# Kernel optimization log

Measured on AMD Instinct MI355X. Metric: run time of the kernel, lower is better.

The kernel has to match this reference:

```python
import jax, jax.numpy as jnp
import numpy as np

N_NODES = 50000
N_EDGES = 600000
IN_CH = 128
HID_CH = 128
OUT_CH = 64
NUM_GRAPHS = 512


def _gcn_conv(x, W, b, src, dst, n):
    # PyG GCNConv (eval): h = D^{-1/2} (A + I) D^{-1/2} (x W) + b
    h = x @ W  # [N, C]
    loop = jnp.arange(n)
    s = jnp.concatenate([src, loop])  # add self-loops
    d = jnp.concatenate([dst, loop])
    deg = jax.ops.segment_sum(jnp.ones_like(d, dtype=h.dtype), d, num_segments=n)
    dinv = jnp.where(deg > 0, jax.lax.rsqrt(deg), 0.0)
    coef = dinv[s] * dinv[d]  # [E+N]
    msg = h[s] * coef[:, None]  # gather + scale
    out = jax.ops.segment_sum(msg, d, num_segments=n)  # scatter-add
    return out + b


def setup_inputs() -> dict:
    key = jax.random.key(0)
    ks = jax.random.split(key, 10)
    x = jax.random.normal(ks[0], (N_NODES, IN_CH), dtype=jnp.float32)
    edge_index = jax.random.randint(ks[1], (2, N_EDGES), 0, N_NODES, dtype=jnp.int64)
    batch = jnp.sort(jax.random.randint(ks[2], (N_NODES,), 0, NUM_GRAPHS, dtype=jnp.int64))
    sc1 = 1.0 / np.sqrt(IN_CH)
    sc2 = 1.0 / np.sqrt(HID_CH)
    W1 = jax.random.uniform(ks[3], (IN_CH, HID_CH), jnp.float32, -sc1, sc1)
    b1 = jnp.zeros((HID_CH,), jnp.float32)
    W2 = jax.random.uniform(ks[4], (HID_CH, HID_CH), jnp.float32, -sc2, sc2)
    b2 = jnp.zeros((HID_CH,), jnp.float32)
    Wlin = jax.random.uniform(ks[5], (HID_CH, OUT_CH), jnp.float32, -sc2, sc2)
    blin = jax.random.uniform(ks[6], (OUT_CH,), jnp.float32, -sc2, sc2)
    return {"x": x, "W1": W1, "b1": b1, "W2": W2, "b2": b2,
            "Wlin": Wlin, "blin": blin, "edge_index": edge_index, "batch": batch}


def reference(x, W1, b1, W2, b2, Wlin, blin, edge_index, batch):
    n = x.shape[0]
    src, dst = edge_index[0], edge_index[1]
    h = jax.nn.relu(_gcn_conv(x, W1, b1, src, dst, n))
    # dropout: identity in eval mode (training=False)
    h = jax.nn.relu(_gcn_conv(h, W2, b2, src, dst, n))
    # global mean pool over graphs
    summed = jax.ops.segment_sum(h, batch, num_segments=NUM_GRAPHS)
    cnt = jax.ops.segment_sum(jnp.ones((n,), h.dtype), batch, num_segments=NUM_GRAPHS)
    pooled = summed / jnp.maximum(cnt, 1.0)[:, None]
    return pooled @ Wlin + blin  # [NUM_GRAPHS, OUT_CH]
```

## Files before the change

kernel.cpp:

```cpp
#include <hip/hip_runtime.h>

#define N_NODES 50000
#define N_EDGES 600000
#define CH 128
#define NUM_GRAPHS 512
#define OUT_CH 64
#define DSH 6
#define DSTRIDE 64

typedef unsigned int uint32;

__device__ __forceinline__ uint32 bfpack(float a, float b) {
    uint32 ua = __builtin_bit_cast(uint32, a);
    uint32 ub = __builtin_bit_cast(uint32, b);
    ua = (ua + 0x7fffu + ((ua >> 16) & 1u)) >> 16;
    ub = (ub + 0x7fffu + ((ub >> 16) & 1u)) >> 16;
    return (ub << 16) | ua;
}
__device__ __forceinline__ float bf_lo(uint32 v) {
    return __builtin_bit_cast(float, v << 16);
}
__device__ __forceinline__ float bf_hi(uint32 v) {
    return __builtin_bit_cast(float, v & 0xffff0000u);
}

__global__ void k_fill_pad(const int* __restrict__ src, const int* __restrict__ dst,
                           int* __restrict__ cur, int* __restrict__ srcs) {
    int e = blockIdx.x * 256 + threadIdx.x;
    if (e < N_EDGES) {
        int s = src[e];
        int d = dst[e];
        int p = atomicAdd(&cur[d], 1);
        srcs[(d << DSH) + p] = s;
    }
}

__global__ void k_dinv(const int* __restrict__ cur, float* __restrict__ dinv) {
    int i = blockIdx.x * 256 + threadIdx.x;
    if (i < N_NODES) dinv[i] = rsqrtf((float)(cur[i] + 1));
}

__global__ __launch_bounds__(256, 2) void k_gemm(const float* __restrict__ A,
                                                 const float* __restrict__ W,
                                                 const float* __restrict__ dinv,
                                                 uint32* __restrict__ outb) {
    __shared__ float ws[CH][CH];
    int tid = threadIdx.x;
    int cg = tid & 7;
    int rg = tid >> 3;
    int row0 = blockIdx.x * 128;

    #pragma unroll
    for (int it = 0; it < 16; ++it) {
        int idx = it * 256 + tid;
        int k = idx >> 5;
        int c4 = (idx & 31) << 2;
        *(float4*)&ws[k][c4] = *(const float4*)&W[k * CH + c4];
    }
    __syncthreads();

    const float* ap[4];
    #pragma unroll
    for (int rr = 0; rr < 4; ++rr) {
        int gr = row0 + rg * 4 + rr;
        ap[rr] = &A[(size_t)min(gr, N_NODES - 1) * CH];
    }

    float acc[4][16];
    #pragma unroll
    for (int i = 0; i < 4; ++i)
        #pragma unroll
        for (int j = 0; j < 16; ++j) acc[i][j] = 0.f;

    for (int kt = 0; kt < CH; kt += 4) {
        float4 a0 = *(const float4*)(ap[0] + kt);
        float4 a1 = *(const float4*)(ap[1] + kt);
        float4 a2 = *(const float4*)(ap[2] + kt);
        float4 a3 = *(const float4*)(ap[3] + kt);
        #pragma unroll
        for (int dk = 0; dk < 4; ++dk) {
            float4 w0 = *(float4*)&ws[kt + dk][cg * 4 + 0];
            float4 w1 = *(float4*)&ws[kt + dk][cg * 4 + 32];
            float4 w2 = *(float4*)&ws[kt + dk][cg * 4 + 64];
            float4 w3 = *(float4*)&ws[kt + dk][cg * 4 + 96];
            float v0 = (dk == 0) ? a0.x : (dk == 1) ? a0.y : (dk == 2) ? a0.z : a0.w;
            float v1 = (dk == 0) ? a1.x : (dk == 1) ? a1.y : (dk == 2) ? a1.z : a1.w;
            float v2 = (dk == 0) ? a2.x : (dk == 1) ? a2.y : (dk == 2) ? a2.z : a2.w;
            float v3 = (dk == 0) ? a3.x : (dk == 1) ? a3.y : (dk == 2) ? a3.z : a3.w;
            acc[0][0]  += v0 * w0.x; acc[0][1]  += v0 * w0.y;
            acc[0][2]  += v0 * w0.z; acc[0][3]  += v0 * w0.w;
            acc[0][4]  += v0 * w1.x; acc[0][5]  += v0 * w1.y;
            acc[0][6]  += v0 * w1.z; acc[0][7]  += v0 * w1.w;
            acc[0][8]  += v0 * w2.x; acc[0][9]  += v0 * w2.y;
            acc[0][10] += v0 * w2.z; acc[0][11] += v0 * w2.w;
            acc[0][12] += v0 * w3.x; acc[0][13] += v0 * w3.y;
            acc[0][14] += v0 * w3.z; acc[0][15] += v0 * w3.w;
            acc[1][0]  += v1 * w0.x; acc[1][1]  += v1 * w0.y;
            acc[1][2]  += v1 * w0.z; acc[1][3]  += v1 * w0.w;
            acc[1][4]  += v1 * w1.x; acc[1][5]  += v1 * w1.y;
            acc[1][6]  += v1 * w1.z; acc[1][7]  += v1 * w1.w;
            acc[1][8]  += v1 * w2.x; acc[1][9]  += v1 * w2.y;
            acc[1][10] += v1 * w2.z; acc[1][11] += v1 * w2.w;
            acc[1][12] += v1 * w3.x; acc[1][13] += v1 * w3.y;
            acc[1][14] += v1 * w3.z; acc[1][15] += v1 * w3.w;
            acc[2][0]  += v2 * w0.x; acc[2][1]  += v2 * w0.y;
            acc[2][2]  += v2 * w0.z; acc[2][3]  += v2 * w0.w;
            acc[2][4]  += v2 * w1.x; acc[2][5]  += v2 * w1.y;
            acc[2][6]  += v2 * w1.z; acc[2][7]  += v2 * w1.w;
            acc[2][8]  += v2 * w2.x; acc[2][9]  += v2 * w2.y;
            acc[2][10] += v2 * w2.z; acc[2][11] += v2 * w2.w;
            acc[2][12] += v2 * w3.x; acc[2][13] += v2 * w3.y;
            acc[2][14] += v2 * w3.z; acc[2][15] += v2 * w3.w;
            acc[3][0]  += v3 * w0.x; acc[3][1]  += v3 * w0.y;
            acc[3][2]  += v3 * w0.z; acc[3][3]  += v3 * w0.w;
            acc[3][4]  += v3 * w1.x; acc[3][5]  += v3 * w1.y;
            acc[3][6]  += v3 * w1.z; acc[3][7]  += v3 * w1.w;
            acc[3][8]  += v3 * w2.x; acc[3][9]  += v3 * w2.y;
            acc[3][10] += v3 * w2.z; acc[3][11] += v3 * w2.w;
            acc[3][12] += v3 * w3.x; acc[3][13] += v3 * w3.y;
            acc[3][14] += v3 * w3.z; acc[3][15] += v3 * w3.w;
        }
    }

    #pragma unroll
    for (int rr = 0; rr < 4; ++rr) {
        int gr = row0 + rg * 4 + rr;
        if (gr < N_NODES) {
            float sc = dinv[gr];
            #pragma unroll
            for (int q = 0; q < 4; ++q) {
                uint32 p0 = bfpack(acc[rr][q * 4 + 0] * sc, acc[rr][q * 4 + 1] * sc);
                uint32 p1 = bfpack(acc[rr][q * 4 + 2] * sc, acc[rr][q * 4 + 3] * sc);
                *(uint2*)&outb[gr * 64 + cg * 2 + q * 16] = make_uint2(p0, p1);
            }
        }
    }
}

__global__ __launch_bounds__(256) void k_agg(const uint32* __restrict__ hb,
                                             const float* __restrict__ dinv,
                                             const int* __restrict__ cnt_arr,
                                             const int* __restrict__ srcs,
                                             const float* __restrict__ bias,
                                             float* __restrict__ out) {
    int node = __builtin_amdgcn_readfirstlane(blockIdx.x * 4 + (threadIdx.x >> 6));
    int lane = threadIdx.x & 63;

    float dn = dinv[node];
    uint32 vs = hb[node * 64 + lane];
    float ax = bf_lo(vs), ay = bf_hi(vs);

    int start = node << DSH;
    int cnt = cnt_arr[node];
    int last = start + cnt - 1;
    for (int j = 0; j < cnt; j += 8) {
        int i0 = start + j;
        int i1 = min(i0 + 1, last);
        int i2 = min(i0 + 2, last);
        int i3 = min(i0 + 3, last);
        int i4 = min(i0 + 4, last);
        int i5 = min(i0 + 5, last);
        int i6 = min(i0 + 6, last);
        int i7 = min(i0 + 7, last);
        int s0 = srcs[i0], s1 = srcs[i1], s2 = srcs[i2], s3 = srcs[i3];
        int s4 = srcs[i4], s5 = srcs[i5], s6 = srcs[i6], s7 = srcs[i7];
        uint32 v0 = hb[s0 * 64 + lane];
        uint32 v1 = hb[s1 * 64 + lane];
        uint32 v2 = hb[s2 * 64 + lane];
        uint32 v3 = hb[s3 * 64 + lane];
        uint32 v4 = hb[s4 * 64 + lane];
        uint32 v5 = hb[s5 * 64 + lane];
        uint32 v6 = hb[s6 * 64 + lane];
        uint32 v7 = hb[s7 * 64 + lane];
        int rem = cnt - j;
        v1 = (rem > 1) ? v1 : 0u;
        v2 = (rem > 2) ? v2 : 0u;
        v3 = (rem > 3) ? v3 : 0u;
        v4 = (rem > 4) ? v4 : 0u;
        v5 = (rem > 5) ? v5 : 0u;
        v6 = (rem > 6) ? v6 : 0u;
        v7 = (rem > 7) ? v7 : 0u;
        ax += bf_lo(v0); ay += bf_hi(v0);
        ax += bf_lo(v1); ay += bf_hi(v1);
        ax += bf_lo(v2); ay += bf_hi(v2);
        ax += bf_lo(v3); ay += bf_hi(v3);
        ax += bf_lo(v4); ay += bf_hi(v4);
        ax += bf_lo(v5); ay += bf_hi(v5);
        ax += bf_lo(v6); ay += bf_hi(v6);
        ax += bf_lo(v7); ay += bf_hi(v7);
    }
    float2 b = ((const float2*)bias)[lane];
    ax = fmaxf(ax * dn + b.x, 0.f);
    ay = fmaxf(ay * dn + b.y, 0.f);
    ((float2*)out)[node * 64 + lane] = make_float2(ax, ay);
}

__global__ __launch_bounds__(256) void k_pool_linear(const float* __restrict__ h,
                                                     const int* __restrict__ batch,
                                                     const float* __restrict__ Wl,
                                                     const float* __restrict__ bl,
                                                     float* __restrict__ out) {
    __shared__ int sb[2];
    __shared__ float4 sacc[256];
    __shared__ float xr[CH];
    __shared__ float po[4][OUT_CH];
    int g = blockIdx.x;
    int tid = threadIdx.x;
    if (tid < 2) {
        int target = g + tid;
        int lo = 0, hi = N_NODES;
        while (lo < hi) {
            int mid = (lo + hi) >> 1;
            if (batch[mid] < target) lo = mid + 1; else hi = mid;
        }
        sb[tid] = lo;
    }
    __syncthreads();
    int lo = sb[0], hi = sb[1];
    int q = tid & 31;
    int r = tid >> 5;
    const float4* h4 = (const float4*)h;
    float4 acc = make_float4(0.f, 0.f, 0.f, 0.f);
    for (int i = lo + r; i < hi; i += 8) {
        float4 v = h4[(size_t)i * 32 + q];
        acc.x += v.x; acc.y += v.y; acc.z += v.z; acc.w += v.w;
    }
    sacc[tid] = acc;
    __syncthreads();
    if (r == 0) {
        #pragma unroll
        for (int p = 1; p < 8; ++p) {
            float4 t = sacc[q + p * 32];
            acc.x += t.x; acc.y += t.y; acc.z += t.z; acc.w += t.w;
        }
        float inv = 1.f / (float)((hi - lo) > 0 ? (hi - lo) : 1);
        xr[q * 4 + 0] = acc.x * inv;
        xr[q * 4 + 1] = acc.y * inv;
        xr[q * 4 + 2] = acc.z * inv;
        xr[q * 4 + 3] = acc.w * inv;
    }
    __syncthreads();
    int c = tid & 63;
    int kh = tid >> 6;
    float o = 0.f;
    #pragma unroll 8
    for (int k = kh * 32; k < kh * 32 + 32; ++k) o += xr[k] * Wl[k * OUT_CH + c];
    po[kh][c] = o;
    __syncthreads();
    if (tid < OUT_CH) {
        float v = bl[tid] + po[0][tid] + po[1][tid] + po[2][tid] + po[3][tid];
        out[g * OUT_CH + tid] = v;
    }
}

extern "C" void kernel_launch(void* const* d_in, const int* in_sizes, int n_in,
                              void* d_out, int out_size, void* d_ws, size_t ws_size,
                              hipStream_t stream) {
    const float* x    = (const float*)d_in[0];
    const float* W1   = (const float*)d_in[1];
    const float* b1   = (const float*)d_in[2];
    const float* W2   = (const float*)d_in[3];
    const float* b2   = (const float*)d_in[4];
    const float* Wlin = (const float*)d_in[5];
    const float* blin = (const float*)d_in[6];
    const int* ei     = (const int*)d_in[7];
    const int* batch  = (const int*)d_in[8];
    const int* esrc = ei;
    const int* edst = ei + N_EDGES;
    float* out = (float*)d_out;

    char* w = (char*)d_ws;
    size_t o = 0;
    float* hA     = (float*)(w + o);  o += (size_t)N_NODES * CH * 4;
    uint32* hb    = (uint32*)(w + o); o += (size_t)N_NODES * 64 * 4;
    int* srcs     = (int*)(w + o);    o += (size_t)N_NODES * DSTRIDE * 4;
    float* dinv   = (float*)(w + o);  o += 200704;
    int* cur      = (int*)(w + o);    o += 200704;
    (void)ws_size; (void)in_sizes; (void)n_in; (void)out_size;

    hipMemsetAsync(cur, 0, N_NODES * sizeof(int), stream);

    dim3 b256(256);
    k_fill_pad<<<dim3((N_EDGES + 255) / 256), b256, 0, stream>>>(esrc, edst, cur, srcs);
    k_dinv<<<dim3((N_NODES + 255) / 256), b256, 0, stream>>>(cur, dinv);

    dim3 gG((N_NODES + 127) / 128);
    dim3 gA(N_NODES / 4);
    k_gemm<<<gG, b256, 0, stream>>>(x, W1, dinv, hb);
    k_agg<<<gA, b256, 0, stream>>>(hb, dinv, cur, srcs, b1, hA);
    k_gemm<<<gG, b256, 0, stream>>>(hA, W2, dinv, hb);
    k_agg<<<gA, b256, 0, stream>>>(hb, dinv, cur, srcs, b2, hA);
    k_pool_linear<<<dim3(NUM_GRAPHS), b256, 0, stream>>>(hA, batch, Wlin, blin, out);
}
```

Before: 238.4 us.

## Use bf16 MFMA for node GEMMs with bf16 inputs and fused degree scaling

Replaces the FP32 FMA-based GEMM with bf16 MFMA 16x16x32 instructions. A is staged in LDS as bf16, and W is pre-transposed to bf16. New kernels cast x to bf16 and prepare transposed bf16 weights. The first aggregation now writes bf16 output for the second GEMM, and the separate dinv kernel is removed by computing rsqrt inline. This cuts FP32 compute and memory traffic, at the cost of lower precision for inputs and weights and extra cast/prep launches.

```diff
diff --git a/kernel.cpp b/kernel.cpp
--- a/kernel.cpp
+++ b/kernel.cpp
@@ -9,6 +9,9 @@
 #define DSTRIDE 64
 
 typedef unsigned int uint32;
+typedef unsigned short ushort16_t;
+typedef __attribute__((ext_vector_type(8))) short short8;
+typedef __attribute__((ext_vector_type(4))) float floatx4;
 
 __device__ __forceinline__ uint32 bfpack(float a, float b) {
     uint32 ua = __builtin_bit_cast(uint32, a);
@@ -16,6 +19,11 @@
     ua = (ua + 0x7fffu + ((ua >> 16) & 1u)) >> 16;
     ub = (ub + 0x7fffu + ((ub >> 16) & 1u)) >> 16;
     return (ub << 16) | ua;
+}
+__device__ __forceinline__ unsigned short bfr(float f) {
+    uint32 u = __builtin_bit_cast(uint32, f);
+    u = (u + 0x7fffu + ((u >> 16) & 1u)) >> 16;
+    return (unsigned short)u;
 }
 __device__ __forceinline__ float bf_lo(uint32 v) {
     return __builtin_bit_cast(float, v << 16);
@@ -35,123 +43,103 @@
     }
 }
 
-__global__ void k_dinv(const int* __restrict__ cur, float* __restrict__ dinv) {
+__global__ void k_cast(const float4* __restrict__ x, uint2* __restrict__ xb, int n4) {
     int i = blockIdx.x * 256 + threadIdx.x;
-    if (i < N_NODES) dinv[i] = rsqrtf((float)(cur[i] + 1));
-}
-
-__global__ __launch_bounds__(256, 2) void k_gemm(const float* __restrict__ A,
-                                                 const float* __restrict__ W,
-                                                 const float* __restrict__ dinv,
-                                                 uint32* __restrict__ outb) {
-    __shared__ float ws[CH][CH];
+    if (i < n4) {
+        float4 v = x[i];
+        xb[i] = make_uint2(bfpack(v.x, v.y), bfpack(v.z, v.w));
+    }
+}
+
+__global__ void k_prep(const float* __restrict__ W1, const float* __restrict__ W2,
+                       unsigned short* __restrict__ W1t, unsigned short* __restrict__ W2t) {
+    int idx = blockIdx.x * 256 + threadIdx.x;
+    int mat = idx >> 14;
+    int rem = idx & 16383;
+    int k = rem >> 7, c = rem & 127;
+    const float* W = mat ? W2 : W1;
+    unsigned short* Wt = mat ? W2t : W1t;
+    Wt[c * 128 + k] = bfr(W[k * 128 + c]);
+}
+
+__global__ __launch_bounds__(256, 2) void k_gemm(const unsigned short* __restrict__ Ab,
+                                                 const unsigned short* __restrict__ Wt,
+                                                 const int* __restrict__ cur,
+                                                 unsigned short* __restrict__ outb) {
+    __shared__ __align__(16) unsigned short as_[128][136];
+    __shared__ __align__(16) unsigned short bs[128][136];
     int tid = threadIdx.x;
-    int cg = tid & 7;
-    int rg = tid >> 3;
     int row0 = blockIdx.x * 128;
 
     #pragma unroll
-    for (int it = 0; it < 16; ++it) {
+    for (int it = 0; it < 8; ++it) {
         int idx = it * 256 + tid;
-        int k = idx >> 5;
-        int c4 = (idx & 31) << 2;
-        *(float4*)&ws[k][c4] = *(const float4*)&W[k * CH + c4];
-    }
-    __syncthreads();
-
-    const float* ap[4];
-    #pragma unroll
-    for (int rr = 0; rr < 4; ++rr) {
-        int gr = row0 + rg * 4 + rr;
-        ap[rr] = &A[(size_t)min(gr, N_NODES - 1) * CH];
-    }
-
-    float acc[4][16];
-    #pragma unroll
-    for (int i = 0; i < 4; ++i)
-        #pragma unroll
-        for (int j = 0; j < 16; ++j) acc[i][j] = 0.f;
-
-    for (int kt = 0; kt < CH; kt += 4) {
-        float4 a0 = *(const float4*)(ap[0] + kt);
-        float4 a1 = *(const float4*)(ap[1] + kt);
-        float4 a2 = *(const float4*)(ap[2] + kt);
-        float4 a3 = *(const float4*)(ap[3] + kt);
-        #pragma unroll
-        for (int dk = 0; dk < 4; ++dk) {
-            float4 w0 = *(float4*)&ws[kt + dk][cg * 4 + 0];
-            float4 w1 = *(float4*)&ws[kt + dk][cg * 4 + 32];
-            float4 w2 = *(float4*)&ws[kt + dk][cg * 4 + 64];
-            float4 w3 = *(float4*)&ws[kt + dk][cg * 4 + 96];
-            float v0 = (dk == 0) ? a0.x : (dk == 1) ? a0.y : (dk == 2) ? a0.z : a0.w;
-            float v1 = (dk == 0) ? a1.x : (dk == 1) ? a1.y : (dk == 2) ? a1.z : a1.w;
-            float v2 = (dk == 0) ? a2.x : (dk == 1) ? a2.y : (dk == 2) ? a2.z : a2.w;
-            float v3 = (dk == 0) ? a3.x : (dk == 1) ? a3.y : (dk == 2) ? a3.z : a3.w;
-            acc[0][0]  += v0 * w0.x; acc[0][1]  += v0 * w0.y;
-            acc[0][2]  += v0 * w0.z; acc[0][3]  += v0 * w0.w;
-            acc[0][4]  += v0 * w1.x; acc[0][5]  += v0 * w1.y;
-            acc[0][6]  += v0 * w1.z; acc[0][7]  += v0 * w1.w;
-            acc[0][8]  += v0 * w2.x; acc[0][9]  += v0 * w2.y;
-            acc[0][10] += v0 * w2.z; acc[0][11] += v0 * w2.w;
-            acc[0][12] += v0 * w3.x; acc[0][13] += v0 * w3.y;
-            acc[0][14] += v0 * w3.z; acc[0][15] += v0 * w3.w;
-            acc[1][0]  += v1 * w0.x; acc[1][1]  += v1 * w0.y;
-            acc[1][2]  += v1 * w0.z; acc[1][3]  += v1 * w0.w;
-            acc[1][4]  += v1 * w1.x; acc[1][5]  += v1 * w1.y;
-            acc[1][6]  += v1 * w1.z; acc[1][7]  += v1 * w1.w;
-            acc[1][8]  += v1 * w2.x; acc[1][9]  += v1 * w2.y;
-            acc[1][10] += v1 * w2.z; acc[1][11] += v1 * w2.w;
-            acc[1][12] += v1 * w3.x; acc[1][13] += v1 * w3.y;
-            acc[1][14] += v1 * w3.z; acc[1][15] += v1 * w3.w;
-            acc[2][0]  += v2 * w0.x; acc[2][1]  += v2 * w0.y;
-            acc[2][2]  += v2 * w0.z; acc[2][3]  += v2 * w0.w;
-            acc[2][4]  += v2 * w1.x; acc[2][5]  += v2 * w1.y;
-            acc[2][6]  += v2 * w1.z; acc[2][7]  += v2 * w1.w;
-            acc[2][8]  += v2 * w2.x; acc[2][9]  += v2 * w2.y;
-            acc[2][10] += v2 * w2.z; acc[2][11] += v2 * w2.w;
-            acc[2][12] += v2 * w3.x; acc[2][13] += v2 * w3.y;
-            acc[2][14] += v2 * w3.z; acc[2][15] += v2 * w3.w;
-            acc[3][0]  += v3 * w0.x; acc[3][1]  += v3 * w0.y;
-            acc[3][2]  += v3 * w0.z; acc[3][3]  += v3 * w0.w;
-            acc[3][4]  += v3 * w1.x; acc[3][5]  += v3 * w1.y;
-            acc[3][6]  += v3 * w1.z; acc[3][7]  += v3 * w1.w;
-            acc[3][8]  += v3 * w2.x; acc[3][9]  += v3 * w2.y;
-            acc[3][10] += v3 * w2.z; acc[3][11] += v3 * w2.w;
-            acc[3][12] += v3 * w3.x; acc[3][13] += v3 * w3.y;
-            acc[3][14] += v3 * w3.z; acc[3][15] += v3 * w3.w;
-        }
-    }
-
-    #pragma unroll
-    for (int rr = 0; rr < 4; ++rr) {
-        int gr = row0 + rg * 4 + rr;
-        if (gr < N_NODES) {
-            float sc = dinv[gr];
-            #pragma unroll
-            for (int q = 0; q < 4; ++q) {
-                uint32 p0 = bfpack(acc[rr][q * 4 + 0] * sc, acc[rr][q * 4 + 1] * sc);
-                uint32 p1 = bfpack(acc[rr][q * 4 + 2] * sc, acc[rr][q * 4 + 3] * sc);
-                *(uint2*)&outb[gr * 64 + cg * 2 + q * 16] = make_uint2(p0, p1);
+        int r = idx >> 4, seg = idx & 15;
+        int gr = min(row0 + r, N_NODES - 1);
+        *(uint4*)&as_[r][seg * 8] = *(const uint4*)&Ab[(size_t)gr * 128 + seg * 8];
+    }
+    #pragma unroll
+    for (int it = 0; it < 8; ++it) {
+        int idx = it * 256 + tid;
+        int c = idx >> 4, seg = idx & 15;
+        *(uint4*)&bs[c][seg * 8] = *(const uint4*)&Wt[c * 128 + seg * 8];
+    }
+    __syncthreads();
+
+    int w = tid >> 6, lane = tid & 63, q = lane >> 4, m = lane & 15;
+    int q8 = q * 8;
+    floatx4 acc[2][8];
+    #pragma unroll
+    for (int rt = 0; rt < 2; ++rt)
+        #pragma unroll
+        for (int ct = 0; ct < 8; ++ct) {
+            floatx4 z = {0.f, 0.f, 0.f, 0.f};
+            acc[rt][ct] = z;
+        }
+
+    #pragma unroll
+    for (int kc = 0; kc < 128; kc += 32) {
+        short8 a0 = *(const short8*)&as_[w * 32 + m][kc + q8];
+        short8 a1 = *(const short8*)&as_[w * 32 + 16 + m][kc + q8];
+        #pragma unroll
+        for (int ct = 0; ct < 8; ++ct) {
+            short8 b = *(const short8*)&bs[ct * 16 + m][kc + q8];
+            acc[0][ct] = __builtin_amdgcn_mfma_f32_16x16x32_bf16(a0, b, acc[0][ct], 0, 0, 0);
+            acc[1][ct] = __builtin_amdgcn_mfma_f32_16x16x32_bf16(a1, b, acc[1][ct], 0, 0, 0);
+        }
+    }
+
+    #pragma unroll
+    for (int rt = 0; rt < 2; ++rt) {
+        #pragma unroll
+        for (int i = 0; i < 4; ++i) {
+            int gr = row0 + w * 32 + rt * 16 + q * 4 + i;
+            if (gr < N_NODES) {
+                float sc = rsqrtf((float)(cur[gr] + 1));
+                #pragma unroll
+                for (int ct = 0; ct < 8; ++ct) {
+                    outb[(size_t)gr * 128 + ct * 16 + m] = bfr(acc[rt][ct][i] * sc);
+                }
             }
         }
     }
 }
 
 __global__ __launch_bounds__(256) void k_agg(const uint32* __restrict__ hb,
-                                             const float* __restrict__ dinv,
                                              const int* __restrict__ cnt_arr,
                                              const int* __restrict__ srcs,
                                              const float* __restrict__ bias,
-                                             float* __restrict__ out) {
+                                             uint32* __restrict__ outB,
+                                             float2* __restrict__ outF) {
     int node = __builtin_amdgcn_readfirstlane(blockIdx.x * 4 + (threadIdx.x >> 6));
     int lane = threadIdx.x & 63;
 
-    float dn = dinv[node];
+    int cnt = cnt_arr[node];
+    float dn = rsqrtf((float)(cnt + 1));
     uint32 vs = hb[node * 64 + lane];
     float ax = bf_lo(vs), ay = bf_hi(vs);
 
     int start = node << DSH;
-    int cnt = cnt_arr[node];
     int last = start + cnt - 1;
     for (int j = 0; j < cnt; j += 8) {
         int i0 = start + j;
@@ -192,7 +180,8 @@
     float2 b = ((const float2*)bias)[lane];
     ax = fmaxf(ax * dn + b.x, 0.f);
     ay = fmaxf(ay * dn + b.y, 0.f);
-    ((float2*)out)[node * 64 + lane] = make_float2(ax, ay);
+    if (outB) outB[node * 64 + lane] = bfpack(ax, ay);
+    if (outF) outF[node * 64 + lane] = make_float2(ax, ay);
 }
 
 __global__ __launch_bounds__(256) void k_pool_linear(const float* __restrict__ h,
@@ -271,24 +260,29 @@
 
     char* w = (char*)d_ws;
     size_t o = 0;
-    float* hA     = (float*)(w + o);  o += (size_t)N_NODES * CH * 4;
-    uint32* hb    = (uint32*)(w + o); o += (size_t)N_NODES * 64 * 4;
-    int* srcs     = (int*)(w + o);    o += (size_t)N_NODES * DSTRIDE * 4;
-    float* dinv   = (float*)(w + o);  o += 200704;
-    int* cur      = (int*)(w + o);    o += 200704;
+    float* hA            = (float*)(w + o);          o += (size_t)N_NODES * CH * 4;
+    unsigned short* hb   = (unsigned short*)(w + o); o += (size_t)N_NODES * CH * 2;
+    uint32* habf         = (uint32*)(w + o);         o += (size_t)N_NODES * 64 * 4;
+    unsigned short* xb   = (unsigned short*)(w + o); o += (size_t)N_NODES * CH * 2;
+    unsigned short* W1t  = (unsigned short*)(w + o); o += 16384 * 2;
+    unsigned short* W2t  = (unsigned short*)(w + o); o += 16384 * 2;
+    int* srcs            = (int*)(w + o);            o += (size_t)N_NODES * DSTRIDE * 4;
+    int* cur             = (int*)(w + o);            o += 200704;
     (void)ws_size; (void)in_sizes; (void)n_in; (void)out_size;
 
     hipMemsetAsync(cur, 0, N_NODES * sizeof(int), stream);
 
     dim3 b256(256);
     k_fill_pad<<<dim3((N_EDGES + 255) / 256), b256, 0, stream>>>(esrc, edst, cur, srcs);
-    k_dinv<<<dim3((N_NODES + 255) / 256), b256, 0, stream>>>(cur, dinv);
+    k_cast<<<dim3(N_NODES * CH / 4 / 256), b256, 0, stream>>>((const float4*)x, (uint2*)xb,
+                                                              N_NODES * CH / 4);
+    k_prep<<<dim3(128), b256, 0, stream>>>(W1, W2, W1t, W2t);
 
     dim3 gG((N_NODES + 127) / 128);
     dim3 gA(N_NODES / 4);
-    k_gemm<<<gG, b256, 0, stream>>>(x, W1, dinv, hb);
-    k_agg<<<gA, b256, 0, stream>>>(hb, dinv, cur, srcs, b1, hA);
-    k_gemm<<<gG, b256, 0, stream>>>(hA, W2, dinv, hb);
-    k_agg<<<gA, b256, 0, stream>>>(hb, dinv, cur, srcs, b2, hA);
+    k_gemm<<<gG, b256, 0, stream>>>(xb, W1t, cur, hb);
+    k_agg<<<gA, b256, 0, stream>>>((const uint32*)hb, cur, srcs, b1, habf, nullptr);
+    k_gemm<<<gG, b256, 0, stream>>>((const unsigned short*)habf, W2t, cur, hb);
+    k_agg<<<gA, b256, 0, stream>>>((const uint32*)hb, cur, srcs, b2, nullptr, (float2*)hA);
     k_pool_linear<<<dim3(NUM_GRAPHS), b256, 0, stream>>>(hA, batch, Wlin, blin, out);
 }
```

Result: faster. 205.0 us (-14.0%).
